# Optimization experiments

Measured on AMD Instinct MI355X. Metric: run time of the kernel, lower is better.

The kernel has to match this reference:

```python
import jax, jax.numpy as jnp
import numpy as np

EMBED_DIM = 1024
NUM_HEADS = 16
HEAD_DIM = EMBED_DIM // NUM_HEADS


def setup_inputs() -> dict:
    key = jax.random.key(0)
    k1, k2, k3, k4, k5 = jax.random.split(key, 5)
    B, S, D = 2, 2048, EMBED_DIM
    s_in = 1.0 / np.sqrt(D)
    x = jax.random.normal(k1, (B, S, D), dtype=jnp.float32)
    W_qkv = jax.random.uniform(k2, (D, 3 * D), dtype=jnp.float32, minval=-s_in, maxval=s_in)
    b_qkv = jax.random.uniform(k3, (3 * D,), dtype=jnp.float32, minval=-s_in, maxval=s_in)
    W_out = jax.random.uniform(k4, (D, D), dtype=jnp.float32, minval=-s_in, maxval=s_in)
    b_out = jax.random.uniform(k5, (D,), dtype=jnp.float32, minval=-s_in, maxval=s_in)
    return {"x": x, "W_qkv": W_qkv, "b_qkv": b_qkv, "W_out": W_out, "b_out": b_out}


def reference(x, W_qkv, b_qkv, W_out, b_out):
    B, S, D = x.shape
    H, Hd = NUM_HEADS, HEAD_DIM
    qkv = x @ W_qkv + b_qkv                      # [B,S,3D]
    qkv = qkv.reshape(B, S, 3, H, Hd)
    q = qkv[:, :, 0].transpose(0, 2, 1, 3)       # [B,H,S,Hd]
    k = qkv[:, :, 1].transpose(0, 2, 1, 3)
    v = qkv[:, :, 2].transpose(0, 2, 1, 3)
    scores = jnp.einsum('bhsd,bhtd->bhst', q, k) / jnp.sqrt(jnp.float32(Hd))
    attn = jax.nn.softmax(scores, axis=-1)       # dropout is identity in eval mode
    out = jnp.einsum('bhst,bhtd->bhsd', attn, v)
    out = out.transpose(0, 2, 1, 3).reshape(B, S, D)
    return out @ W_out + b_out
```

## Files before the change

kernel.cpp:

```cpp
#include <hip/hip_runtime.h>
#include <stdint.h>
#include <math.h>

#define EMBED 1024
#define HEADS 16
#define HDIM  64
#define SEQ   2048
#define BATCH 2

typedef __bf16 bf16x8 __attribute__((ext_vector_type(8)));
typedef float  f32x4  __attribute__((ext_vector_type(4)));
typedef unsigned short u16x8 __attribute__((ext_vector_type(8)));
typedef unsigned short u16x4 __attribute__((ext_vector_type(4)));
typedef uint32_t u32x4v __attribute__((ext_vector_type(4)));

static __device__ __forceinline__ unsigned short f2bf(float f){
  union { float f; uint32_t u; } v; v.f = f;
  uint32_t u = v.u;
  uint32_t r = (u + 0x7FFFu + ((u >> 16) & 1u)) >> 16;
  return (unsigned short)r;
}
static __device__ __forceinline__ bf16x8 as_bf(u16x8 v){ return __builtin_bit_cast(bf16x8, v); }

static __device__ __forceinline__ uint32_t pk_bf16(float a, float b){
#if defined(__has_builtin) && __has_builtin(__builtin_amdgcn_cvt_pk_bf16_f32)
  typedef __bf16 bf16x2 __attribute__((ext_vector_type(2)));
  bf16x2 p = __builtin_amdgcn_cvt_pk_bf16_f32(a, b);
  return __builtin_bit_cast(uint32_t, p);
#else
  return (uint32_t)f2bf(a) | ((uint32_t)f2bf(b) << 16);
#endif
}

static __device__ __forceinline__ float fexp2(float x){
#if defined(__has_builtin) && __has_builtin(__builtin_amdgcn_exp2f)
  return __builtin_amdgcn_exp2f(x);
#else
  return exp2f(x);
#endif
}

static __device__ __forceinline__ void stage16(const unsigned short* gp,
                                               unsigned short* lp_wave, int lane){
#if defined(__has_builtin) && __has_builtin(__builtin_amdgcn_global_load_lds)
  __builtin_amdgcn_global_load_lds((const __attribute__((address_space(1))) void*)gp,
                                   (__attribute__((address_space(3))) void*)lp_wave,
                                   16, 0, 0);
#else
  *(u16x8*)(lp_wave + lane * 8) = *(const u16x8*)gp;
#endif
}

__global__ __launch_bounds__(256) void prep(
    const float* __restrict__ x,      unsigned short* __restrict__ xb,
    const float* __restrict__ W_qkv,  unsigned short* __restrict__ wqkvT,
    const float* __restrict__ W_out,  unsigned short* __restrict__ woutT)
{
  __shared__ unsigned short T[32 * 36];
  const int bid = blockIdx.x;
  const int t   = threadIdx.x;

  if (bid < 4096){
    int i = (bid * 256 + t) * 4;
    float4 v = *(const float4*)(x + i);
    u16x4 o;
    o[0] = f2bf(v.x); o[1] = f2bf(v.y); o[2] = f2bf(v.z); o[3] = f2bf(v.w);
    *(u16x4*)(xb + i) = o;
    return;
  }
  const float* W; unsigned short* Wt; int N, n0, k0;
  if (bid < 7168){
    int idx = bid - 4096;
    W = W_qkv; Wt = wqkvT; N = 3072;
    n0 = (idx % 96) * 32; k0 = (idx / 96) * 32;
  } else {
    int idx = bid - 7168;
    W = W_out; Wt = woutT; N = 1024;
    n0 = (idx & 31) * 32; k0 = (idx >> 5) * 32;
  }
  int kr = t >> 3, nc = (t & 7) * 4;
  float4 wv = *(const float4*)(W + (size_t)(k0 + kr) * N + n0 + nc);
  T[(nc + 0) * 36 + kr] = f2bf(wv.x);
  T[(nc + 1) * 36 + kr] = f2bf(wv.y);
  T[(nc + 2) * 36 + kr] = f2bf(wv.z);
  T[(nc + 3) * 36 + kr] = f2bf(wv.w);
  __syncthreads();
  int nr = t >> 3, kc = (t & 7) * 4;
  *(u16x4*)(Wt + (size_t)(n0 + nr) * 1024 + k0 + kc) = *(const u16x4*)&T[nr * 36 + kc];
}

__global__ __launch_bounds__(256) void gemm_qkv(
    const unsigned short* __restrict__ A,
    const unsigned short* __restrict__ Bt,
    const float* __restrict__ bias,
    unsigned short* __restrict__ q_ws,
    unsigned short* __restrict__ k_ws,
    unsigned short* __restrict__ vt_ws,
    int M, int N, int K)
{
  __shared__ unsigned short As[128 * 32];
  __shared__ unsigned short Bs[128 * 32];
  const int tid  = threadIdx.x;
  const int bm   = blockIdx.y, bn = blockIdx.x;
  const int w    = tid >> 6, lane = tid & 63;
  const int quad = lane >> 4, l16 = lane & 15;
  const int wm   = (w >> 1) * 64, wn = (w & 1) * 64;

  f32x4 acc[4][4] = {};

  for (int k0 = 0; k0 < K; k0 += 32) {
    #pragma unroll
    for (int i = 0; i < 2; i++){
      int c = w + i * 4;
      int row = c * 16 + (lane >> 2);
      int kg = (lane & 3) ^ (row & 3);
      stage16(A  + (size_t)(bm * 128 + row) * K + k0 + kg * 8, &As[c * 512], lane);
      stage16(Bt + (size_t)(bn * 128 + row) * K + k0 + kg * 8, &Bs[c * 512], lane);
    }
    __syncthreads();

    bf16x8 af[4], bfr[4];
    #pragma unroll
    for (int t = 0; t < 4; t++){
      int ra = wm + t * 16 + l16;
      int rb = wn + t * 16 + l16;
      af[t]  = as_bf(*(const u16x8*)&As[(ra << 5) + ((quad ^ (ra & 3)) << 3)]);
      bfr[t] = as_bf(*(const u16x8*)&Bs[(rb << 5) + ((quad ^ (rb & 3)) << 3)]);
    }
    #pragma unroll
    for (int mt = 0; mt < 4; mt++)
      #pragma unroll
      for (int nt = 0; nt < 4; nt++)
        acc[mt][nt] = __builtin_amdgcn_mfma_f32_16x16x32_bf16(af[mt], bfr[nt], acc[mt][nt], 0, 0, 0);
    __syncthreads();
  }

  const int which = (bn * 128) >> 10;

  if (which == 2){
    unsigned short* T = (w < 2) ? &As[w * 2048] : &Bs[(w - 2) * 2048];
    const int h = (bn - 16) * 2 + (wn >> 6);
    const size_t bhbase = ((size_t)((bm >> 4) * HEADS + h)) * HDIM * SEQ;
    const int sgbase = (bm & 15) * 128 + wm;
    #pragma unroll
    for (int p = 0; p < 2; p++){
      #pragma unroll
      for (int mi = 0; mi < 2; mi++){
        int mt = p * 2 + mi;
        #pragma unroll
        for (int nt = 0; nt < 4; nt++){
          float bv = bias[bn * 128 + wn + nt * 16 + l16];
          uint32_t lo = pk_bf16(acc[mt][nt][0] + bv, acc[mt][nt][1] + bv);
          uint32_t hi = pk_bf16(acc[mt][nt][2] + bv, acc[mt][nt][3] + bv);
          int hd = nt * 16 + l16;
          int qc = (quad * 2 + mi) ^ (hd & 7);
          uint32_t* d2 = (uint32_t*)&T[hd * 32 + qc * 4];
          d2[0] = lo; d2[1] = hi;
        }
      }
      #pragma unroll
      for (int i = 0; i < 4; i++){
        int id = i * 64 + lane;
        int hd = id >> 2, ch = id & 3;
        int q0 = (ch * 2) ^ (hd & 7), q1 = (ch * 2 + 1) ^ (hd & 7);
        const uint32_t* s0p = (const uint32_t*)&T[hd * 32 + q0 * 4];
        const uint32_t* s1p = (const uint32_t*)&T[hd * 32 + q1 * 4];
        u32x4v st; st[0] = s0p[0]; st[1] = s0p[1]; st[2] = s1p[0]; st[3] = s1p[1];
        *(u32x4v*)(vt_ws + bhbase + (size_t)hd * SEQ + sgbase + p * 32 + ch * 8) = st;
      }
    }
  } else {
    unsigned short* dst = (which == 0) ? q_ws : k_ws;
    const float scale = (which == 0) ? 0.18033688f : 1.0f;
    const int b = bm >> 4;
    #pragma unroll
    for (int nt = 0; nt < 4; nt++){
      int gnb = bn * 128 + wn + nt * 16;
      int h   = (gnb & 1023) >> 6;
      int hd  = (gnb & 63) + l16;
      float bv = bias[gnb + l16];
      unsigned short* dp = dst + (size_t)(b * HEADS + h) * SEQ * HDIM + hd;
      #pragma unroll
      for (int mt = 0; mt < 4; mt++){
        int s0 = ((bm & 15) * 128) + wm + mt * 16 + quad * 4;
        #pragma unroll
        for (int r = 0; r < 4; r++)
          dp[(size_t)(s0 + r) * HDIM] = f2bf((acc[mt][nt][r] + bv) * scale);
      }
    }
  }
}

__global__ __launch_bounds__(256) void gemm_out(
    const unsigned short* __restrict__ A,
    const unsigned short* __restrict__ Bt,
    const float* __restrict__ bias,
    float* __restrict__ Cout,
    int M, int N, int K)
{
  __shared__ unsigned short As[128 * 32];
  __shared__ unsigned short Bs[64 * 32];
  const int tid  = threadIdx.x;
  const int bm   = blockIdx.y, bn = blockIdx.x;
  const int w    = tid >> 6, lane = tid & 63;
  const int quad = lane >> 4, l16 = lane & 15;
  const int wm   = (w >> 1) * 64, wn = (w & 1) * 32;

  f32x4 acc[4][2] = {};

  for (int k0 = 0; k0 < K; k0 += 32) {
    #pragma unroll
    for (int i = 0; i < 2; i++){
      int c = w + i * 4;
      int row = c * 16 + (lane >> 2);
      int kg = (lane & 3) ^ (row & 3);
      stage16(A + (size_t)(bm * 128 + row) * K + k0 + kg * 8, &As[c * 512], lane);
    }
    {
      int c = w;
      int row = c * 16 + (lane >> 2);
      int kg = (lane & 3) ^ (row & 3);
      stage16(Bt + (size_t)(bn * 64 + row) * K + k0 + kg * 8, &Bs[c * 512], lane);
    }
    __syncthreads();

    bf16x8 af[4], bfr[2];
    #pragma unroll
    for (int t = 0; t < 4; t++){
      int ra = wm + t * 16 + l16;
      af[t] = as_bf(*(const u16x8*)&As[(ra << 5) + ((quad ^ (ra & 3)) << 3)]);
    }
    #pragma unroll
    for (int t = 0; t < 2; t++){
      int rb = wn + t * 16 + l16;
      bfr[t] = as_bf(*(const u16x8*)&Bs[(rb << 5) + ((quad ^ (rb & 3)) << 3)]);
    }
    #pragma unroll
    for (int mt = 0; mt < 4; mt++)
      #pragma unroll
      for (int nt = 0; nt < 2; nt++)
        acc[mt][nt] = __builtin_amdgcn_mfma_f32_16x16x32_bf16(af[mt], bfr[nt], acc[mt][nt], 0, 0, 0);
    __syncthreads();
  }

  #pragma unroll
  for (int mt = 0; mt < 4; mt++)
    #pragma unroll
    for (int nt = 0; nt < 2; nt++)
      #pragma unroll
      for (int r = 0; r < 4; r++){
        int gm = bm * 128 + wm + mt * 16 + quad * 4 + r;
        int gn = bn * 64 + wn + nt * 16 + l16;
        Cout[(size_t)gm * N + gn] = acc[mt][nt][r] + bias[gn];
      }
}

__global__ __launch_bounds__(512) void attn(
    const unsigned short* __restrict__ q_ws,
    const unsigned short* __restrict__ k_ws,
    const unsigned short* __restrict__ vt_ws,
    unsigned short* __restrict__ o_ws)
{
  __shared__ unsigned short Qs[256 * 64];
  __shared__ unsigned short Ks[2][64 * 64];
  __shared__ unsigned short VTs[2][64 * 64];
  const int tid  = threadIdx.x;
  const int qt   = blockIdx.x, bh = blockIdx.y;
  const int w    = tid >> 6, lane = tid & 63;
  const int quad = lane >> 4, l16 = lane & 15;
  const size_t base = (size_t)bh * SEQ * HDIM;

  #pragma unroll
  for (int i = 0; i < 4; i++){
    int c = w * 4 + i;
    int row = c * 8 + (lane >> 3);
    int kg = (lane & 7) ^ (row & 7);
    stage16(q_ws + base + (size_t)(qt * 256 + row) * HDIM + kg * 8, &Qs[c * 512], lane);
  }

  const int srow = w * 8 + (lane >> 3);
  const int skg  = (lane & 7) ^ (srow & 7);
  const int dofs = w * 512 + lane * 8;

  stage16(k_ws  + base + (size_t)srow * HDIM + skg * 8, &Ks[0][w * 512],  lane);
  stage16(vt_ws + base + (size_t)srow * SEQ + skg * 8,  &VTs[0][w * 512], lane);
  __syncthreads();

  bf16x8 bq[2][2];
  #pragma unroll
  for (int mq = 0; mq < 2; mq++){
    int row = w * 32 + mq * 16 + l16;
    #pragma unroll
    for (int ks = 0; ks < 2; ks++)
      bq[mq][ks] = as_bf(*(const u16x8*)&Qs[(row << 6) + ((((ks << 2) + quad) ^ (row & 7)) << 3)]);
  }

  const unsigned short* kp = k_ws  + base + (size_t)(64 + srow) * HDIM + skg * 8;
  const unsigned short* vp = vt_ws + base + (size_t)srow * SEQ + 64 + skg * 8;

  f32x4 acc[2][4] = {};
  float li[2] = {0.f, 0.f};

  for (int kt2 = 0; kt2 < SEQ / 128; kt2++){
    #pragma unroll
    for (int half = 0; half < 2; half++){
      const int cur = half;
      const int kt  = kt2 * 2 + half;
      u16x8 kpre, vpre;
      if (kt < SEQ / 64 - 1){
        kpre = *(const u16x8*)kp;  kp += 64 * HDIM;
        vpre = *(const u16x8*)vp;  vp += 64;
      }

      f32x4 sf[4][2] = {};
      #pragma unroll
      for (int ks = 0; ks < 2; ks++){
        #pragma unroll
        for (int nt = 0; nt < 4; nt++){
          int rk = nt * 16 + l16;
          bf16x8 ak = as_bf(*(const u16x8*)&Ks[cur][(rk << 6) + ((((ks << 2) + quad) ^ (rk & 7)) << 3)]);
          #pragma unroll
          for (int mq = 0; mq < 2; mq++)
            sf[nt][mq] = __builtin_amdgcn_mfma_f32_16x16x32_bf16(ak, bq[mq][ks], sf[nt][mq], 0, 0, 0);
        }
      }

      #pragma unroll
      for (int nt = 0; nt < 4; nt++)
        #pragma unroll
        for (int mq = 0; mq < 2; mq++)
          #pragma unroll
          for (int r = 0; r < 4; r++)
            sf[nt][mq][r] = fexp2(sf[nt][mq][r]);
      #pragma unroll
      for (int mq = 0; mq < 2; mq++)
        #pragma unroll
        for (int nt = 0; nt < 4; nt++)
          li[mq] += (sf[nt][mq][0] + sf[nt][mq][1]) + (sf[nt][mq][2] + sf[nt][mq][3]);

      #pragma unroll
      for (int c = 0; c < 2; c++){
        bf16x8 ap[2];
        #pragma unroll
        for (int mq = 0; mq < 2; mq++){
          u32x4v aw;
          aw[0] = pk_bf16(sf[c * 2][mq][0],     sf[c * 2][mq][1]);
          aw[1] = pk_bf16(sf[c * 2][mq][2],     sf[c * 2][mq][3]);
          aw[2] = pk_bf16(sf[c * 2 + 1][mq][0], sf[c * 2 + 1][mq][1]);
          aw[3] = pk_bf16(sf[c * 2 + 1][mq][2], sf[c * 2 + 1][mq][3]);
          ap[mq] = __builtin_bit_cast(bf16x8, aw);
        }
        #pragma unroll
        for (int nt = 0; nt < 4; nt++){
          int rv = nt * 16 + l16;
          bf16x8 bv = as_bf(*(const u16x8*)&VTs[cur][(rv << 6) + ((((c << 2) + quad) ^ (rv & 7)) << 3)]);
          #pragma unroll
          for (int mq = 0; mq < 2; mq++)
            acc[mq][nt] = __builtin_amdgcn_mfma_f32_16x16x32_bf16(ap[mq], bv, acc[mq][nt], 0, 0, 0);
        }
      }

      if (kt < SEQ / 64 - 1){
        *(u16x8*)&Ks[cur ^ 1][dofs]  = kpre;
        *(u16x8*)&VTs[cur ^ 1][dofs] = vpre;
      }
      __syncthreads();
    }
  }

  #pragma unroll
  for (int mq = 0; mq < 2; mq++){
    li[mq] += __shfl_xor(li[mq], 16);
    li[mq] += __shfl_xor(li[mq], 32);
  }
  float inv[2] = {1.0f / li[0], 1.0f / li[1]};
  float invr[2][4];
  #pragma unroll
  for (int mq = 0; mq < 2; mq++)
    #pragma unroll
    for (int r = 0; r < 4; r++)
      invr[mq][r] = __shfl(inv[mq], quad * 4 + r);

  int b = bh >> 4, h = bh & 15;
  #pragma unroll
  for (int mq = 0; mq < 2; mq++)
    #pragma unroll
    for (int nt = 0; nt < 4; nt++)
      #pragma unroll
      for (int r = 0; r < 4; r++){
        int s = qt * 256 + w * 32 + mq * 16 + quad * 4 + r;
        int d = h * 64 + nt * 16 + l16;
        o_ws[((size_t)(b * SEQ + s)) * EMBED + d] = f2bf(acc[mq][nt][r] * invr[mq][r]);
      }
}

extern "C" void kernel_launch(void* const* d_in, const int* in_sizes, int n_in,
                              void* d_out, int out_size, void* d_ws, size_t ws_size,
                              hipStream_t stream) {
  const float* x     = (const float*)d_in[0];
  const float* W_qkv = (const float*)d_in[1];
  const float* b_qkv = (const float*)d_in[2];
  const float* W_out = (const float*)d_in[3];
  const float* b_out = (const float*)d_in[4];
  float* out = (float*)d_out;

  char* ws = (char*)d_ws;
  unsigned short* xb    = (unsigned short*)(ws);
  unsigned short* q     = (unsigned short*)(ws + ((size_t)8  << 20));
  unsigned short* k     = (unsigned short*)(ws + ((size_t)16 << 20));
  unsigned short* vt    = (unsigned short*)(ws + ((size_t)24 << 20));
  unsigned short* wqkvT = (unsigned short*)(ws + ((size_t)32 << 20));
  unsigned short* woutT = (unsigned short*)(ws + ((size_t)38 << 20));
  unsigned short* o     = xb;

  prep<<<dim3(8192), dim3(256), 0, stream>>>(x, xb, W_qkv, wqkvT, W_out, woutT);

  gemm_qkv<<<dim3(24, 32), dim3(256), 0, stream>>>(
      xb, wqkvT, b_qkv, q, k, vt, 4096, 3072, 1024);

  attn<<<dim3(8, 32), dim3(512), 0, stream>>>(q, k, vt, o);

  gemm_out<<<dim3(16, 32), dim3(256), 0, stream>>>(
      o, woutT, b_out, out, 4096, 1024, 1024);
}
```

Baseline: 204.1 us.

## Vectorize QKV epilogue stores via swapped MFMA operands and swap grid ordering

For the Q/K tiles, the MFMA operands are swapped so each lane holds four consecutive head-dim values. The epilogue can then write packed 8-byte bf16 stores instead of scattered 2-byte stores. The V-transpose path drops its LDS staging and writes 4-element vectors straight to global memory. Both GEMMs also swap block-index mapping so consecutive blocks walk along M, which changes L2 reuse of weight tiles, but the direct V stores are narrower than the previous 16-byte ones.

```diff
diff --git a/kernel.cpp b/kernel.cpp
--- a/kernel.cpp
+++ b/kernel.cpp
@@ -101,10 +101,12 @@
   __shared__ unsigned short As[128 * 32];
   __shared__ unsigned short Bs[128 * 32];
   const int tid  = threadIdx.x;
-  const int bm   = blockIdx.y, bn = blockIdx.x;
+  const int bm   = blockIdx.x, bn = blockIdx.y;
   const int w    = tid >> 6, lane = tid & 63;
   const int quad = lane >> 4, l16 = lane & 15;
   const int wm   = (w >> 1) * 64, wn = (w & 1) * 64;
+  const int which = (bn * 128) >> 10;
+  const bool isV  = (which == 2);
 
   f32x4 acc[4][4] = {};
 
@@ -127,65 +129,62 @@
       af[t]  = as_bf(*(const u16x8*)&As[(ra << 5) + ((quad ^ (ra & 3)) << 3)]);
       bfr[t] = as_bf(*(const u16x8*)&Bs[(rb << 5) + ((quad ^ (rb & 3)) << 3)]);
     }
-    #pragma unroll
-    for (int mt = 0; mt < 4; mt++)
-      #pragma unroll
-      for (int nt = 0; nt < 4; nt++)
-        acc[mt][nt] = __builtin_amdgcn_mfma_f32_16x16x32_bf16(af[mt], bfr[nt], acc[mt][nt], 0, 0, 0);
+    if (isV){
+      #pragma unroll
+      for (int mt = 0; mt < 4; mt++)
+        #pragma unroll
+        for (int nt = 0; nt < 4; nt++)
+          acc[mt][nt] = __builtin_amdgcn_mfma_f32_16x16x32_bf16(af[mt], bfr[nt], acc[mt][nt], 0, 0, 0);
+    } else {
+      #pragma unroll
+      for (int mt = 0; mt < 4; mt++)
+        #pragma unroll
+        for (int nt = 0; nt < 4; nt++)
+          acc[mt][nt] = __builtin_amdgcn_mfma_f32_16x16x32_bf16(bfr[nt], af[mt], acc[mt][nt], 0, 0, 0);
+    }
     __syncthreads();
   }
 
-  const int which = (bn * 128) >> 10;
-
-  if (which == 2){
-    unsigned short* T = (w < 2) ? &As[w * 2048] : &Bs[(w - 2) * 2048];
+  const int b = bm >> 4;
+
+  if (isV){
     const int h = (bn - 16) * 2 + (wn >> 6);
-    const size_t bhbase = ((size_t)((bm >> 4) * HEADS + h)) * HDIM * SEQ;
-    const int sgbase = (bm & 15) * 128 + wm;
-    #pragma unroll
-    for (int p = 0; p < 2; p++){
-      #pragma unroll
-      for (int mi = 0; mi < 2; mi++){
-        int mt = p * 2 + mi;
-        #pragma unroll
-        for (int nt = 0; nt < 4; nt++){
-          float bv = bias[bn * 128 + wn + nt * 16 + l16];
-          uint32_t lo = pk_bf16(acc[mt][nt][0] + bv, acc[mt][nt][1] + bv);
-          uint32_t hi = pk_bf16(acc[mt][nt][2] + bv, acc[mt][nt][3] + bv);
-          int hd = nt * 16 + l16;
-          int qc = (quad * 2 + mi) ^ (hd & 7);
-          uint32_t* d2 = (uint32_t*)&T[hd * 32 + qc * 4];
-          d2[0] = lo; d2[1] = hi;
-        }
-      }
-      #pragma unroll
-      for (int i = 0; i < 4; i++){
-        int id = i * 64 + lane;
-        int hd = id >> 2, ch = id & 3;
-        int q0 = (ch * 2) ^ (hd & 7), q1 = (ch * 2 + 1) ^ (hd & 7);
-        const uint32_t* s0p = (const uint32_t*)&T[hd * 32 + q0 * 4];
-        const uint32_t* s1p = (const uint32_t*)&T[hd * 32 + q1 * 4];
-        u32x4v st; st[0] = s0p[0]; st[1] = s0p[1]; st[2] = s1p[0]; st[3] = s1p[1];
-        *(u32x4v*)(vt_ws + bhbase + (size_t)hd * SEQ + sgbase + p * 32 + ch * 8) = st;
+    const size_t bhbase = (size_t)(b * HEADS + h) * HDIM * SEQ;
+    #pragma unroll
+    for (int mt = 0; mt < 4; mt++){
+      int s32 = (bm & 15) * 128 + wm + (mt >> 1) * 32;
+      int pos = quad * 8 + (mt & 1) * 4;
+      #pragma unroll
+      for (int nt = 0; nt < 4; nt++){
+        int hd = nt * 16 + l16;
+        float bv = bias[bn * 128 + wn + nt * 16 + l16];
+        uint32_t p0 = pk_bf16(acc[mt][nt][0] + bv, acc[mt][nt][1] + bv);
+        uint32_t p1 = pk_bf16(acc[mt][nt][2] + bv, acc[mt][nt][3] + bv);
+        u16x4 st;
+        st[0] = (unsigned short)p0; st[1] = (unsigned short)(p0 >> 16);
+        st[2] = (unsigned short)p1; st[3] = (unsigned short)(p1 >> 16);
+        *(u16x4*)(vt_ws + bhbase + (size_t)hd * SEQ + s32 + pos) = st;
       }
     }
   } else {
     unsigned short* dst = (which == 0) ? q_ws : k_ws;
     const float scale = (which == 0) ? 0.18033688f : 1.0f;
-    const int b = bm >> 4;
     #pragma unroll
     for (int nt = 0; nt < 4; nt++){
       int gnb = bn * 128 + wn + nt * 16;
       int h   = (gnb & 1023) >> 6;
-      int hd  = (gnb & 63) + l16;
-      float bv = bias[gnb + l16];
-      unsigned short* dp = dst + (size_t)(b * HEADS + h) * SEQ * HDIM + hd;
+      int hd0 = (gnb & 63) + quad * 4;
+      float4 b4 = *(const float4*)&bias[gnb + quad * 4];
+      size_t rowbase = (size_t)(b * HEADS + h) * SEQ;
       #pragma unroll
       for (int mt = 0; mt < 4; mt++){
-        int s0 = ((bm & 15) * 128) + wm + mt * 16 + quad * 4;
-        #pragma unroll
-        for (int r = 0; r < 4; r++)
-          dp[(size_t)(s0 + r) * HDIM] = f2bf((acc[mt][nt][r] + bv) * scale);
+        int s = (bm & 15) * 128 + wm + mt * 16 + l16;
+        uint32_t p0 = pk_bf16((acc[mt][nt][0] + b4.x) * scale, (acc[mt][nt][1] + b4.y) * scale);
+        uint32_t p1 = pk_bf16((acc[mt][nt][2] + b4.z) * scale, (acc[mt][nt][3] + b4.w) * scale);
+        u16x4 st;
+        st[0] = (unsigned short)p0; st[1] = (unsigned short)(p0 >> 16);
+        st[2] = (unsigned short)p1; st[3] = (unsigned short)(p1 >> 16);
+        *(u16x4*)(dst + (rowbase + s) * HDIM + hd0) = st;
       }
     }
   }
@@ -201,7 +200,7 @@
   __shared__ unsigned short As[128 * 32];
   __shared__ unsigned short Bs[64 * 32];
   const int tid  = threadIdx.x;
-  const int bm   = blockIdx.y, bn = blockIdx.x;
+  const int bm   = blockIdx.x, bn = blockIdx.y;
   const int w    = tid >> 6, lane = tid & 63;
   const int quad = lane >> 4, l16 = lane & 15;
   const int wm   = (w >> 1) * 64, wn = (w & 1) * 32;
@@ -415,11 +414,11 @@
 
   prep<<<dim3(8192), dim3(256), 0, stream>>>(x, xb, W_qkv, wqkvT, W_out, woutT);
 
-  gemm_qkv<<<dim3(24, 32), dim3(256), 0, stream>>>(
+  gemm_qkv<<<dim3(32, 24), dim3(256), 0, stream>>>(
       xb, wqkvT, b_qkv, q, k, vt, 4096, 3072, 1024);
 
   attn<<<dim3(8, 32), dim3(512), 0, stream>>>(q, k, vt, o);
 
-  gemm_out<<<dim3(16, 32), dim3(256), 0, stream>>>(
+  gemm_out<<<dim3(32, 16), dim3(256), 0, stream>>>(
       o, woutT, b_out, out, 4096, 1024, 1024);
 }
```

Measured after the change: 215.5 us. +5.6%, slower.
